# Performance work log

Hardware: AMD Instinct MI355X
Metric: run time of the kernel (lower is better)

The kernel has to match this reference:

```python
import jax, jax.numpy as jnp
import numpy as np

DIM = 256
WINDOW = 8
HEADS = 8
N = WINDOW * WINDOW


def _make_rpb_index(window_size: int) -> jnp.ndarray:
    hs = np.arange(window_size)
    coords = np.stack(np.meshgrid(hs, hs, indexing='ij'))  # [2, w, w]
    flat = coords.reshape(2, -1)                            # [2, N]
    rel = flat[:, :, None] - flat[:, None, :]               # [2, N, N]
    rel = rel.transpose(1, 2, 0).copy()                     # [N, N, 2]
    rel[:, :, 0] += window_size - 1
    rel[:, :, 1] += window_size - 1
    rel[:, :, 0] *= 2 * window_size - 1
    return jnp.asarray(rel.sum(-1), dtype=jnp.int32)        # [N, N]


def setup_inputs() -> dict:
    key = jax.random.key(0)
    k_x, k_qw, k_qb, k_pw, k_pb, k_rpb = jax.random.split(key, 6)
    B_ = 2048
    x = jax.random.normal(k_x, (B_, N, DIM), dtype=jnp.float32)
    mask = jnp.zeros((64, N, N), dtype=jnp.float32)
    # nn.Linear weights stored [out, in] as in torch
    qkv_w = jax.random.normal(k_qw, (3 * DIM, DIM), dtype=jnp.float32) * 0.02
    qkv_b = jnp.zeros((3 * DIM,), dtype=jnp.float32)
    proj_w = jax.random.normal(k_pw, (DIM, DIM), dtype=jnp.float32) * 0.02
    proj_b = jnp.zeros((DIM,), dtype=jnp.float32)
    rpb_table = jax.random.normal(k_rpb, ((2 * WINDOW - 1) ** 2, HEADS), dtype=jnp.float32) * 0.02
    rpb_index = _make_rpb_index(WINDOW)
    return {"x": x, "mask": mask, "qkv_w": qkv_w, "qkv_b": qkv_b,
            "proj_w": proj_w, "proj_b": proj_b, "rpb_table": rpb_table,
            "rpb_index": rpb_index}


def reference(x, mask, qkv_w, qkv_b, proj_w, proj_b, rpb_table, rpb_index):
    B_, n, C = x.shape
    H = HEADS
    d = C // H
    scale = d ** -0.5
    qkv = x @ qkv_w.T + qkv_b                      # [B, N, 3C]
    qkv = qkv.reshape(B_, n, 3, H, d)
    q = qkv[:, :, 0].transpose(0, 2, 1, 3)          # [B, H, N, d]
    k = qkv[:, :, 1].transpose(0, 2, 1, 3)
    v = qkv[:, :, 2].transpose(0, 2, 1, 3)
    attn = jnp.einsum('bhnd,bhmd->bhnm', q * scale, k)
    rpb = rpb_table[rpb_index]                      # [N, N, H]
    attn = attn + rpb.transpose(2, 0, 1)[None]      # [B, H, N, N]
    nW = mask.shape[0]
    attn = attn.reshape(B_ // nW, nW, H, n, n) + mask[None, :, None]
    attn = attn.reshape(B_, H, n, n)
    attn = jax.nn.softmax(attn, axis=-1)
    out = jnp.einsum('bhnm,bhmd->bhnd', attn, v)    # [B, H, N, d]
    out = out.transpose(0, 2, 1, 3).reshape(B_, n, C)
    return out @ proj_w.T + proj_b
```

## Files before the change

kernel.cpp:

```cpp
#include <hip/hip_runtime.h>
#include <hip/hip_bf16.h>


#define TOK 64
#define CDIM 256

typedef __attribute__((ext_vector_type(8))) short short8;
typedef __attribute__((ext_vector_type(4))) float f32x4;
typedef __attribute__((ext_vector_type(4))) float float4_t;

__device__ __forceinline__ short f2bf(float f) {
  union { float f; unsigned u; } v; v.f = f;
  unsigned r = v.u + 0x7FFFu + ((v.u >> 16) & 1u);
  return (short)(r >> 16);
}

__device__ __forceinline__ unsigned cvt2(float a, float b) {
  union { __hip_bfloat162 h; unsigned u; } v;
  v.h = __float22bfloat162_rn(make_float2(a, b));
  return v.u;
}

__device__ __forceinline__ short8 pack88(f32x4 lo, f32x4 hi) {
  union { short8 s; unsigned u[4]; } r;
  r.u[0] = cvt2(lo[0], lo[1]);
  r.u[1] = cvt2(lo[2], lo[3]);
  r.u[2] = cvt2(hi[0], hi[1]);
  r.u[3] = cvt2(hi[2], hi[3]);
  return r.s;
}

__global__ void preconv_kernel(const float* __restrict__ qkv_w,
                               const float* __restrict__ proj_w,
                               const float* __restrict__ rpb_table,
                               const int* __restrict__ rpb_index,
                               const float* __restrict__ mask,
                               short* __restrict__ wqkv,
                               short* __restrict__ wproj,
                               float* __restrict__ rpbP,
                               float* __restrict__ maskP) {
  int idx = blockIdx.x * blockDim.x + threadIdx.x;
  const float scale = 0.17677669529663687f;
  const int NW1 = 768 * 256;
  const int NW2 = NW1 + 256 * 256;
  const int NW3 = NW2 + 8 * 64 * 64;
  const int NW4 = NW3 + 64 * 64 * 64;
  if (idx < NW1) {
    float v = qkv_w[idx];
    if (idx < 256 * 256) v *= scale;
    wqkv[idx] = f2bf(v);
  } else if (idx < NW2) {
    int i = idx - NW1;
    wproj[i] = f2bf(proj_w[i]);
  } else if (idx < NW3) {
    int i = idx - NW2;
    int h = i >> 12;
    int pos = i & 4095;
    int kt = pos >> 6;
    int t = pos & 63;
    int llv = t >> 2, ni = t & 3;
    int q = ni * 16 + llv;
    rpbP[i] = rpb_table[rpb_index[q * 64 + kt] * 8 + h];
  } else if (idx < NW4) {
    int i = idx - NW3;
    int win = i >> 12;
    int pos = i & 4095;
    int kt = pos >> 6;
    int t = pos & 63;
    int llv = t >> 2, ni = t & 3;
    int q = ni * 16 + llv;
    maskP[i] = mask[win * 4096 + q * 64 + kt];
  }
}

__global__ void __launch_bounds__(256) xconv_kernel(
    const float* __restrict__ x, float* out) {
  int idx = blockIdx.x * blockDim.x + threadIdx.x;
  int row = idx >> 3;
  int seg = idx & 7;
  const float4_t* s4 = reinterpret_cast<const float4_t*>(
      x + (size_t)row * 256 + seg * 32);
  char* dst = reinterpret_cast<char*>(out) + (size_t)row * 1024 + 512 + seg * 64;
#pragma unroll
  for (int j = 0; j < 4; ++j)
    *reinterpret_cast<short8*>(dst + j * 16) = pack88(s4[2 * j], s4[2 * j + 1]);
}

__global__ void __launch_bounds__(64, 2) attn_kernel(
    const float* __restrict__ qkv_b, const short* __restrict__ wqkv,
    const float* __restrict__ rpbP, const float* __restrict__ maskP,
    float* out) {
  const int bid = blockIdx.x;
  const int sid = (bid & 7) * 2048 + (bid >> 3);
  const int w = sid >> 3;
  const int h = sid & 7;
  const int lane = threadIdx.x & 63;
  const int lg = lane >> 4;
  const int ll = lane & 15;
  const float scale = 0.17677669529663687f;

  const char* xb = reinterpret_cast<const char*>(out) + (size_t)w * TOK * 1024 + 512;

  f32x4 aqk[4][4] = {};
  f32x4 av[4][2] = {};
#pragma unroll 2
  for (int ks = 0; ks < 8; ++ks) {
    const int k0 = ks * 32 + lg * 8;
    short8 xf[4];
#pragma unroll
    for (int ni = 0; ni < 4; ++ni)
      xf[ni] = *reinterpret_cast<const short8*>(
          xb + (size_t)(ni * 16 + ll) * 1024 + k0 * 2);
#pragma unroll
    for (int j = 0; j < 4; ++j) {
      const int cbase = (j >> 1) * 256 + h * 32 + (j & 1) * 16;
      short8 wf = *reinterpret_cast<const short8*>(wqkv + (cbase + ll) * 256 + k0);
#pragma unroll
      for (int ni = 0; ni < 4; ++ni)
        aqk[ni][j] = __builtin_amdgcn_mfma_f32_16x16x32_bf16(wf, xf[ni], aqk[ni][j], 0, 0, 0);
    }
#pragma unroll
    for (int hf = 0; hf < 2; ++hf) {
      short8 wv = *reinterpret_cast<const short8*>(
          wqkv + (512 + h * 32 + hf * 16 + ll) * 256 + k0);
#pragma unroll
      for (int mi = 0; mi < 4; ++mi)
        av[mi][hf] = __builtin_amdgcn_mfma_f32_16x16x32_bf16(xf[mi], wv, av[mi][hf], 0, 0, 0);
    }
  }

  f32x4 bj[4];
#pragma unroll
  for (int j = 0; j < 4; ++j) {
    float4_t t = *reinterpret_cast<const float4_t*>(
        qkv_b + (j >> 1) * 256 + h * 32 + (j & 1) * 16 + lg * 4);
    bj[j] = (j < 2) ? t * scale : t;
  }
  short8 aq[4], bk[4];
#pragma unroll
  for (int ni = 0; ni < 4; ++ni) {
    aq[ni] = pack88(aqk[ni][0] + bj[0], aqk[ni][1] + bj[1]);
    bk[ni] = pack88(aqk[ni][2] + bj[2], aqk[ni][3] + bj[3]);
  }

  short8 vf[2][2];
#pragma unroll
  for (int hf = 0; hf < 2; ++hf) {
    float bb = qkv_b[512 + h * 32 + hf * 16 + ll];
    f32x4 b4{bb, bb, bb, bb};
    vf[hf][0] = pack88(av[0][hf] + b4, av[1][hf] + b4);
    vf[hf][1] = pack88(av[2][hf] + b4, av[3][hf] + b4);
  }

  f32x4 sa[4][4];
  {
    f32x4 z{0.0f, 0.0f, 0.0f, 0.0f};
#pragma unroll
    for (int mi = 0; mi < 4; ++mi)
#pragma unroll
      for (int ni = 0; ni < 4; ++ni)
        sa[mi][ni] = __builtin_amdgcn_mfma_f32_16x16x32_bf16(bk[mi], aq[ni], z, 0, 0, 0);
    const float4_t* rp4 = reinterpret_cast<const float4_t*>(rpbP) + h * 1024;
    const float4_t* mk4 = reinterpret_cast<const float4_t*>(maskP) + (w & 63) * 1024;
#pragma unroll
    for (int mi = 0; mi < 4; ++mi)
#pragma unroll
      for (int r = 0; r < 4; ++r) {
        int kt = mi * 16 + lg * 4 + r;
        float4_t f = rp4[kt * 16 + ll];
        float4_t g = mk4[kt * 16 + ll];
#pragma unroll
        for (int ni = 0; ni < 4; ++ni)
          sa[mi][ni][r] += f[ni] + g[ni];
      }
  }

  float rinv[4];
#pragma unroll
  for (int ni = 0; ni < 4; ++ni) {
    float m = sa[0][ni][0];
#pragma unroll
    for (int mi = 0; mi < 4; ++mi)
#pragma unroll
      for (int r = 0; r < 4; ++r) m = fmaxf(m, sa[mi][ni][r]);
    m = fmaxf(m, __shfl_xor(m, 16));
    m = fmaxf(m, __shfl_xor(m, 32));
    float s = 0.f;
#pragma unroll
    for (int mi = 0; mi < 4; ++mi)
#pragma unroll
      for (int r = 0; r < 4; ++r) {
        float e = __expf(sa[mi][ni][r] - m);
        sa[mi][ni][r] = e;
        s += e;
      }
    s += __shfl_xor(s, 16);
    s += __shfl_xor(s, 32);
    rinv[ni] = 1.0f / s;
  }

  f32x4 oa[2][4] = {};
#pragma unroll
  for (int ni = 0; ni < 4; ++ni) {
    short8 pf0 = pack88(sa[0][ni], sa[1][ni]);
    short8 pf1 = pack88(sa[2][ni], sa[3][ni]);
#pragma unroll
    for (int hf = 0; hf < 2; ++hf) {
      oa[hf][ni] = __builtin_amdgcn_mfma_f32_16x16x32_bf16(vf[hf][0], pf0, oa[hf][ni], 0, 0, 0);
      oa[hf][ni] = __builtin_amdgcn_mfma_f32_16x16x32_bf16(vf[hf][1], pf1, oa[hf][ni], 0, 0, 0);
    }
  }

  char* ob = reinterpret_cast<char*>(out) + (size_t)w * TOK * 1024;
#pragma unroll
  for (int hf = 0; hf < 2; ++hf)
#pragma unroll
    for (int ni = 0; ni < 4; ++ni) {
      f32x4 v = oa[hf][ni] * rinv[ni];
      int q = ni * 16 + ll;
      union { unsigned long long q64; unsigned u[2]; } pk;
      pk.u[0] = cvt2(v[0], v[1]);
      pk.u[1] = cvt2(v[2], v[3]);
      *reinterpret_cast<unsigned long long*>(
          ob + (size_t)q * 1024 + h * 64 + hf * 32 + lg * 8) = pk.q64;
    }
}

__global__ void __launch_bounds__(256, 3) proj_kernel(
    const short* __restrict__ wproj, const float* __restrict__ proj_b,
    float* out) {
  const int bid = blockIdx.x;
  const int t = (bid & 7) * 256 + (bid >> 3);
  const int wv = threadIdx.x >> 6;
  const int lane = threadIdx.x & 63;
  const int lg = lane >> 4;
  const int ll = lane & 15;
  const char* ab = reinterpret_cast<const char*>(out) + (size_t)t * TOK * 1024;

  f32x4 pa[4][4] = {};
#pragma unroll
  for (int ks = 0; ks < 8; ++ks) {
    const int k0 = ks * 32 + lg * 8;
    short8 af[4];
#pragma unroll
    for (int ni = 0; ni < 4; ++ni)
      af[ni] = *reinterpret_cast<const short8*>(
          ab + (size_t)(ni * 16 + ll) * 1024 + k0 * 2);
#pragma unroll
    for (int jj = 0; jj < 4; ++jj) {
      short8 wf = *reinterpret_cast<const short8*>(
          wproj + (wv * 64 + jj * 16 + ll) * 256 + k0);
#pragma unroll
      for (int ni = 0; ni < 4; ++ni)
        pa[jj][ni] = __builtin_amdgcn_mfma_f32_16x16x32_bf16(wf, af[ni], pa[jj][ni], 0, 0, 0);
    }
  }
  __syncthreads();

  float* op = out + (size_t)t * TOK * CDIM;
#pragma unroll
  for (int jj = 0; jj < 4; ++jj) {
    int oc0 = wv * 64 + jj * 16 + lg * 4;
    float4_t pb = *reinterpret_cast<const float4_t*>(proj_b + oc0);
#pragma unroll
    for (int ni = 0; ni < 4; ++ni) {
      f32x4 v = pa[jj][ni] + pb;
      *reinterpret_cast<float4_t*>(op + (ni * 16 + ll) * 256 + oc0) = v;
    }
  }
}

extern "C" void kernel_launch(void* const* d_in, const int* in_sizes, int n_in,
                              void* d_out, int out_size, void* d_ws, size_t ws_size,
                              hipStream_t stream) {
  const float* x        = (const float*)d_in[0];
  const float* mask     = (const float*)d_in[1];
  const float* qkv_w    = (const float*)d_in[2];
  const float* qkv_b    = (const float*)d_in[3];
  const float* proj_w   = (const float*)d_in[4];
  const float* proj_b   = (const float*)d_in[5];
  const float* rpb_tab  = (const float*)d_in[6];
  const int*   rpb_idx  = (const int*)d_in[7];
  float* out = (float*)d_out;

  short* wqkv  = (short*)d_ws;
  short* wproj = wqkv + 768 * 256;
  float* rpbP  = (float*)(wproj + 256 * 256);
  float* maskP = rpbP + 8 * 64 * 64;

  int total = 768 * 256 + 256 * 256 + 8 * 64 * 64 + 64 * 64 * 64;
  preconv_kernel<<<(total + 255) / 256, 256, 0, stream>>>(
      qkv_w, proj_w, rpb_tab, rpb_idx, mask, wqkv, wproj, rpbP, maskP);

  int B = in_sizes[0] / (TOK * CDIM);
  xconv_kernel<<<B * TOK * 8 / 256, 256, 0, stream>>>(x, out);
  attn_kernel<<<B * 8, 64, 0, stream>>>(qkv_b, wqkv, rpbP, maskP, out);
  proj_kernel<<<B, 256, 0, stream>>>(wproj, proj_b, out);
}
```

Measured before the change: 296.6 us.

## Merge x conversion into prep kernel, split QK/V projection loops, raise attn occupancy

Folds the x fp32-to-bf16 conversion into the weight/bias preconversion kernel, which removes one launch. The attention kernel's fused QK and V projection loop is split into two sequential scoped loops so fewer accumulators are live at once, and launch bounds are raised from 2 to 3 waves per SIMD. s_setprio is wrapped around the MFMA bursts to favour matrix issue. The cost is reading the x tile twice from global/L2, with a risk of spills under the tighter register budget.

```diff
diff --git a/kernel.cpp b/kernel.cpp
--- a/kernel.cpp
+++ b/kernel.cpp
@@ -30,15 +30,13 @@
   return r.s;
 }
 
-__global__ void preconv_kernel(const float* __restrict__ qkv_w,
-                               const float* __restrict__ proj_w,
-                               const float* __restrict__ rpb_table,
-                               const int* __restrict__ rpb_index,
-                               const float* __restrict__ mask,
-                               short* __restrict__ wqkv,
-                               short* __restrict__ wproj,
-                               float* __restrict__ rpbP,
-                               float* __restrict__ maskP) {
+__global__ void __launch_bounds__(256) prep_kernel(
+    const float* __restrict__ qkv_w, const float* __restrict__ proj_w,
+    const float* __restrict__ rpb_table, const int* __restrict__ rpb_index,
+    const float* __restrict__ mask, const float* __restrict__ x,
+    short* __restrict__ wqkv, short* __restrict__ wproj,
+    float* __restrict__ rpbP, float* __restrict__ maskP,
+    float* out, int nrow) {
   int idx = blockIdx.x * blockDim.x + threadIdx.x;
   const float scale = 0.17677669529663687f;
   const int NW1 = 768 * 256;
@@ -70,23 +68,22 @@
     int llv = t >> 2, ni = t & 3;
     int q = ni * 16 + llv;
     maskP[i] = mask[win * 4096 + q * 64 + kt];
-  }
-}
-
-__global__ void __launch_bounds__(256) xconv_kernel(
-    const float* __restrict__ x, float* out) {
-  int idx = blockIdx.x * blockDim.x + threadIdx.x;
-  int row = idx >> 3;
-  int seg = idx & 7;
-  const float4_t* s4 = reinterpret_cast<const float4_t*>(
-      x + (size_t)row * 256 + seg * 32);
-  char* dst = reinterpret_cast<char*>(out) + (size_t)row * 1024 + 512 + seg * 64;
-#pragma unroll
-  for (int j = 0; j < 4; ++j)
-    *reinterpret_cast<short8*>(dst + j * 16) = pack88(s4[2 * j], s4[2 * j + 1]);
-}
-
-__global__ void __launch_bounds__(64, 2) attn_kernel(
+  } else {
+    int i = idx - NW4;
+    int row = i >> 3;
+    if (row < nrow) {
+      int seg = i & 7;
+      const float4_t* s4 = reinterpret_cast<const float4_t*>(
+          x + (size_t)row * 256 + seg * 32);
+      char* dst = reinterpret_cast<char*>(out) + (size_t)row * 1024 + 512 + seg * 64;
+#pragma unroll
+      for (int j = 0; j < 4; ++j)
+        *reinterpret_cast<short8*>(dst + j * 16) = pack88(s4[2 * j], s4[2 * j + 1]);
+    }
+  }
+}
+
+__global__ void __launch_bounds__(64, 3) attn_kernel(
     const float* __restrict__ qkv_b, const short* __restrict__ wqkv,
     const float* __restrict__ rpbP, const float* __restrict__ maskP,
     float* out) {
@@ -101,65 +98,79 @@
 
   const char* xb = reinterpret_cast<const char*>(out) + (size_t)w * TOK * 1024 + 512;
 
-  f32x4 aqk[4][4] = {};
-  f32x4 av[4][2] = {};
+  short8 aq[4], bk[4];
+  {
+    f32x4 aqk[4][4] = {};
 #pragma unroll 2
-  for (int ks = 0; ks < 8; ++ks) {
-    const int k0 = ks * 32 + lg * 8;
-    short8 xf[4];
-#pragma unroll
-    for (int ni = 0; ni < 4; ++ni)
-      xf[ni] = *reinterpret_cast<const short8*>(
-          xb + (size_t)(ni * 16 + ll) * 1024 + k0 * 2);
+    for (int ks = 0; ks < 8; ++ks) {
+      const int k0 = ks * 32 + lg * 8;
+      short8 xf[4];
+#pragma unroll
+      for (int ni = 0; ni < 4; ++ni)
+        xf[ni] = *reinterpret_cast<const short8*>(
+            xb + (size_t)(ni * 16 + ll) * 1024 + k0 * 2);
+#pragma unroll
+      for (int j = 0; j < 4; ++j) {
+        const int cbase = (j >> 1) * 256 + h * 32 + (j & 1) * 16;
+        short8 wf = *reinterpret_cast<const short8*>(wqkv + (cbase + ll) * 256 + k0);
+#pragma unroll
+        for (int ni = 0; ni < 4; ++ni)
+          aqk[ni][j] = __builtin_amdgcn_mfma_f32_16x16x32_bf16(wf, xf[ni], aqk[ni][j], 0, 0, 0);
+      }
+    }
+    f32x4 bj[4];
 #pragma unroll
     for (int j = 0; j < 4; ++j) {
-      const int cbase = (j >> 1) * 256 + h * 32 + (j & 1) * 16;
-      short8 wf = *reinterpret_cast<const short8*>(wqkv + (cbase + ll) * 256 + k0);
-#pragma unroll
-      for (int ni = 0; ni < 4; ++ni)
-        aqk[ni][j] = __builtin_amdgcn_mfma_f32_16x16x32_bf16(wf, xf[ni], aqk[ni][j], 0, 0, 0);
+      float4_t t = *reinterpret_cast<const float4_t*>(
+          qkv_b + (j >> 1) * 256 + h * 32 + (j & 1) * 16 + lg * 4);
+      bj[j] = (j < 2) ? t * scale : t;
+    }
+#pragma unroll
+    for (int ni = 0; ni < 4; ++ni) {
+      aq[ni] = pack88(aqk[ni][0] + bj[0], aqk[ni][1] + bj[1]);
+      bk[ni] = pack88(aqk[ni][2] + bj[2], aqk[ni][3] + bj[3]);
+    }
+  }
+
+  short8 vf[2][2];
+  {
+    f32x4 av[4][2] = {};
+#pragma unroll 2
+    for (int ks = 0; ks < 8; ++ks) {
+      const int k0 = ks * 32 + lg * 8;
+      short8 xf[4];
+#pragma unroll
+      for (int mi = 0; mi < 4; ++mi)
+        xf[mi] = *reinterpret_cast<const short8*>(
+            xb + (size_t)(mi * 16 + ll) * 1024 + k0 * 2);
+#pragma unroll
+      for (int hf = 0; hf < 2; ++hf) {
+        short8 wv = *reinterpret_cast<const short8*>(
+            wqkv + (512 + h * 32 + hf * 16 + ll) * 256 + k0);
+#pragma unroll
+        for (int mi = 0; mi < 4; ++mi)
+          av[mi][hf] = __builtin_amdgcn_mfma_f32_16x16x32_bf16(xf[mi], wv, av[mi][hf], 0, 0, 0);
+      }
     }
 #pragma unroll
     for (int hf = 0; hf < 2; ++hf) {
-      short8 wv = *reinterpret_cast<const short8*>(
-          wqkv + (512 + h * 32 + hf * 16 + ll) * 256 + k0);
-#pragma unroll
-      for (int mi = 0; mi < 4; ++mi)
-        av[mi][hf] = __builtin_amdgcn_mfma_f32_16x16x32_bf16(xf[mi], wv, av[mi][hf], 0, 0, 0);
-    }
-  }
-
-  f32x4 bj[4];
-#pragma unroll
-  for (int j = 0; j < 4; ++j) {
-    float4_t t = *reinterpret_cast<const float4_t*>(
-        qkv_b + (j >> 1) * 256 + h * 32 + (j & 1) * 16 + lg * 4);
-    bj[j] = (j < 2) ? t * scale : t;
-  }
-  short8 aq[4], bk[4];
-#pragma unroll
-  for (int ni = 0; ni < 4; ++ni) {
-    aq[ni] = pack88(aqk[ni][0] + bj[0], aqk[ni][1] + bj[1]);
-    bk[ni] = pack88(aqk[ni][2] + bj[2], aqk[ni][3] + bj[3]);
-  }
-
-  short8 vf[2][2];
-#pragma unroll
-  for (int hf = 0; hf < 2; ++hf) {
-    float bb = qkv_b[512 + h * 32 + hf * 16 + ll];
-    f32x4 b4{bb, bb, bb, bb};
-    vf[hf][0] = pack88(av[0][hf] + b4, av[1][hf] + b4);
-    vf[hf][1] = pack88(av[2][hf] + b4, av[3][hf] + b4);
+      float bb = qkv_b[512 + h * 32 + hf * 16 + ll];
+      f32x4 b4{bb, bb, bb, bb};
+      vf[hf][0] = pack88(av[0][hf] + b4, av[1][hf] + b4);
+      vf[hf][1] = pack88(av[2][hf] + b4, av[3][hf] + b4);
+    }
   }
 
   f32x4 sa[4][4];
   {
     f32x4 z{0.0f, 0.0f, 0.0f, 0.0f};
+    __builtin_amdgcn_s_setprio(1);
 #pragma unroll
     for (int mi = 0; mi < 4; ++mi)
 #pragma unroll
       for (int ni = 0; ni < 4; ++ni)
         sa[mi][ni] = __builtin_amdgcn_mfma_f32_16x16x32_bf16(bk[mi], aq[ni], z, 0, 0, 0);
+    __builtin_amdgcn_s_setprio(0);
     const float4_t* rp4 = reinterpret_cast<const float4_t*>(rpbP) + h * 1024;
     const float4_t* mk4 = reinterpret_cast<const float4_t*>(maskP) + (w & 63) * 1024;
 #pragma unroll
@@ -204,11 +215,13 @@
   for (int ni = 0; ni < 4; ++ni) {
     short8 pf0 = pack88(sa[0][ni], sa[1][ni]);
     short8 pf1 = pack88(sa[2][ni], sa[3][ni]);
+    __builtin_amdgcn_s_setprio(1);
 #pragma unroll
     for (int hf = 0; hf < 2; ++hf) {
       oa[hf][ni] = __builtin_amdgcn_mfma_f32_16x16x32_bf16(vf[hf][0], pf0, oa[hf][ni], 0, 0, 0);
       oa[hf][ni] = __builtin_amdgcn_mfma_f32_16x16x32_bf16(vf[hf][1], pf1, oa[hf][ni], 0, 0, 0);
     }
+    __builtin_amdgcn_s_setprio(0);
   }
 
   char* ob = reinterpret_cast<char*>(out) + (size_t)w * TOK * 1024;
@@ -288,12 +301,13 @@
   float* rpbP  = (float*)(wproj + 256 * 256);
   float* maskP = rpbP + 8 * 64 * 64;
 
-  int total = 768 * 256 + 256 * 256 + 8 * 64 * 64 + 64 * 64 * 64;
-  preconv_kernel<<<(total + 255) / 256, 256, 0, stream>>>(
-      qkv_w, proj_w, rpb_tab, rpb_idx, mask, wqkv, wproj, rpbP, maskP);
-
   int B = in_sizes[0] / (TOK * CDIM);
-  xconv_kernel<<<B * TOK * 8 / 256, 256, 0, stream>>>(x, out);
+  int nrow = B * TOK;
+  int total = 768 * 256 + 256 * 256 + 8 * 64 * 64 + 64 * 64 * 64 + nrow * 8;
+  prep_kernel<<<(total + 255) / 256, 256, 0, stream>>>(
+      qkv_w, proj_w, rpb_tab, rpb_idx, mask, x, wqkv, wproj, rpbP, maskP,
+      out, nrow);
+
   attn_kernel<<<B * 8, 64, 0, stream>>>(qkv_b, wqkv, rpbP, maskP, out);
   proj_kernel<<<B, 256, 0, stream>>>(wproj, proj_b, out);
 }
```

Measured after the change: 355.9 us. +20.0%, slower.
